# Kernel tuning notes

Measured on AMD Instinct MI355X. Metric: run time of the kernel, lower is better.

## Reference

```python
import jax, jax.numpy as jnp
import numpy as np

B, L, DG, H = 32, 1024, 1024, 1024  # batch, label_size (=n_graphs), graph dim, hidden

def setup_inputs() -> dict:
    key = jax.random.key(0)
    k1, k2, k3 = jax.random.split(key, 3)
    graph_repr = jax.random.normal(k1, (B, L, DG), dtype=jnp.float32)
    query = jax.random.normal(k2, (B, H), dtype=jnp.float32)
    W = jax.random.normal(k3, (H, L), dtype=jnp.float32) * (1.0 / np.sqrt(H))
    b = jnp.zeros((L,), dtype=jnp.float32)
    return {"graph_repr": graph_repr, "query": query, "W": W, "b": b}

def reference(graph_repr, query, W, b):
    # gate = Sigmoid(Linear(query)) : [B, L]
    gate = jax.nn.sigmoid(query @ W + b)
    # diag_embed(gate) @ graph_repr == per-row scale (same math, no O(L^2) matmul)
    scaled = gate[:, :, None] * graph_repr            # [B, L, DG]
    q_exp = jnp.broadcast_to(query[:, None, :], (query.shape[0], graph_repr.shape[1], query.shape[1]))
    return jnp.concatenate([scaled, q_exp], axis=-1)  # [B, L, DG+H]
```

## Files before the change

kernel.cpp:

```cpp
#include <hip/hip_runtime.h>

#define BB 32
#define LL 1024
#define DGG 1024
#define HH 1024

__global__ __launch_bounds__(256) void gate_kernel(
    const float* __restrict__ query,
    const float* __restrict__ W,
    const float* __restrict__ bias,
    float* __restrict__ gate)
{
    __shared__ float qs[HH];
    __shared__ float partial[4][64];

    const int b  = blockIdx.y;
    const int l0 = blockIdx.x * 64;
    const int t  = threadIdx.x;
    const int ll = t & 63;
    const int hg = t >> 6;

    for (int h = t; h < HH; h += 256)
        qs[h] = query[b * HH + h];
    __syncthreads();

    const int l = l0 + ll;
    const float* Wp = W + (size_t)(hg * 256) * LL + l;
    float sum = 0.f;
    #pragma unroll 8
    for (int h = 0; h < 256; ++h)
        sum += qs[hg * 256 + h] * Wp[(size_t)h * LL];

    partial[hg][ll] = sum;
    __syncthreads();

    if (t < 64) {
        float s = partial[0][t] + partial[1][t] + partial[2][t] + partial[3][t]
                + bias[l0 + t];
        gate[b * LL + l0 + t] = 1.0f / (1.0f + __expf(-s));
    }
}

__global__ __launch_bounds__(256) void out_kernel(
    const float* __restrict__ graph,
    const float* __restrict__ query,
    const float* __restrict__ gate,
    float* __restrict__ out)
{
    const int bl = blockIdx.x;
    const int b  = bl >> 10;
    const int t  = threadIdx.x;
    const float g = gate[bl];

    const float4* gsrc = reinterpret_cast<const float4*>(graph) + (size_t)bl * 256;
    const float4* qsrc = reinterpret_cast<const float4*>(query) + (size_t)b  * 256;
    float4*       dst  = reinterpret_cast<float4*>(out)         + (size_t)bl * 512;

    float4 v = gsrc[t];
    float4 r = make_float4(v.x * g, v.y * g, v.z * g, v.w * g);
    dst[t] = r;
    dst[256 + t] = qsrc[t];
}

extern "C" void kernel_launch(void* const* d_in, const int* in_sizes, int n_in,
                              void* d_out, int out_size, void* d_ws, size_t ws_size,
                              hipStream_t stream) {
    const float* graph = (const float*)d_in[0];
    const float* query = (const float*)d_in[1];
    const float* W     = (const float*)d_in[2];
    const float* bias  = (const float*)d_in[3];
    float* out  = (float*)d_out;
    float* gate = (float*)d_ws;

    dim3 g1(LL / 64, BB);
    gate_kernel<<<g1, 256, 0, stream>>>(query, W, bias, gate);
    out_kernel<<<BB * LL, 256, 0, stream>>>(graph, query, gate, out);
}
```

Before: 377.3 us.

## Fuse gate GEMV and scaled concat output into a single kernel

Merges the gate computation and the output write into one kernel: each block computes 16 gate values for one batch row in shared memory, then streams 16 graph rows, scales them and writes them along with the replicated query. This removes the second launch and the gate round-trip through global memory, and keeps query in registers for the concat half. In exchange, W is re-read per block with only 16-column-wide coalesced segments, and the GEMV is serialized in front of the streaming phase inside every block. Grid ordering puts batch on x, so blocks that share a W column slice run close together, which may help the W reads hit in cache.

After: 377.4 us. No clear change (+0.0%).

```diff
diff --git a/kernel.cpp b/kernel.cpp
--- a/kernel.cpp
+++ b/kernel.cpp
@@ -5,61 +5,56 @@
 #define DGG 1024
 #define HH 1024
 
-__global__ __launch_bounds__(256) void gate_kernel(
+__global__ __launch_bounds__(256) void fused_kernel(
+    const float* __restrict__ graph,
     const float* __restrict__ query,
     const float* __restrict__ W,
     const float* __restrict__ bias,
-    float* __restrict__ gate)
+    float* __restrict__ out)
 {
     __shared__ float qs[HH];
-    __shared__ float partial[4][64];
+    __shared__ float partial[16][16];
+    __shared__ float gate_s[16];
 
-    const int b  = blockIdx.y;
-    const int l0 = blockIdx.x * 64;
+    const int b  = blockIdx.x;
+    const int l0 = blockIdx.y * 16;
     const int t  = threadIdx.x;
-    const int ll = t & 63;
-    const int hg = t >> 6;
 
-    for (int h = t; h < HH; h += 256)
-        qs[h] = query[b * HH + h];
+    const float4* q4p = reinterpret_cast<const float4*>(query + (size_t)b * HH);
+    float4 q4 = q4p[t];
+    reinterpret_cast<float4*>(qs)[t] = q4;
     __syncthreads();
 
-    const int l = l0 + ll;
-    const float* Wp = W + (size_t)(hg * 256) * LL + l;
+    const int j  = t & 15;
+    const int hg = t >> 4;
+    const float* Wbase = W + l0 + j;
     float sum = 0.f;
     #pragma unroll 8
-    for (int h = 0; h < 256; ++h)
-        sum += qs[hg * 256 + h] * Wp[(size_t)h * LL];
-
-    partial[hg][ll] = sum;
+    for (int i = 0; i < 64; ++i) {
+        const int h = hg * 64 + ((i + hg * 4) & 63);
+        sum += qs[h] * Wbase[(size_t)h * LL];
+    }
+    partial[hg][j] = sum;
     __syncthreads();
 
-    if (t < 64) {
-        float s = partial[0][t] + partial[1][t] + partial[2][t] + partial[3][t]
-                + bias[l0 + t];
-        gate[b * LL + l0 + t] = 1.0f / (1.0f + __expf(-s));
+    if (t < 16) {
+        float s = bias[l0 + t];
+        #pragma unroll
+        for (int k = 0; k < 16; ++k) s += partial[k][t];
+        gate_s[t] = 1.0f / (1.0f + __expf(-s));
     }
-}
+    __syncthreads();
 
-__global__ __launch_bounds__(256) void out_kernel(
-    const float* __restrict__ graph,
-    const float* __restrict__ query,
-    const float* __restrict__ gate,
-    float* __restrict__ out)
-{
-    const int bl = blockIdx.x;
-    const int b  = bl >> 10;
-    const int t  = threadIdx.x;
-    const float g = gate[bl];
-
-    const float4* gsrc = reinterpret_cast<const float4*>(graph) + (size_t)bl * 256;
-    const float4* qsrc = reinterpret_cast<const float4*>(query) + (size_t)b  * 256;
-    float4*       dst  = reinterpret_cast<float4*>(out)         + (size_t)bl * 512;
-
-    float4 v = gsrc[t];
-    float4 r = make_float4(v.x * g, v.y * g, v.z * g, v.w * g);
-    dst[t] = r;
-    dst[256 + t] = qsrc[t];
+    const float4* g4 = reinterpret_cast<const float4*>(graph) + ((size_t)b * LL + l0) * 256;
+    float4*       o4 = reinterpret_cast<float4*>(out)         + ((size_t)b * LL + l0) * 512;
+    #pragma unroll 4
+    for (int r = 0; r < 16; ++r) {
+        const float g = gate_s[r];
+        float4 v = g4[(size_t)r * 256 + t];
+        float4 sv = make_float4(v.x * g, v.y * g, v.z * g, v.w * g);
+        o4[(size_t)r * 512 + t]       = sv;
+        o4[(size_t)r * 512 + 256 + t] = q4;
+    }
 }
 
 extern "C" void kernel_launch(void* const* d_in, const int* in_sizes, int n_in,
@@ -69,10 +64,8 @@
     const float* query = (const float*)d_in[1];
     const float* W     = (const float*)d_in[2];
     const float* bias  = (const float*)d_in[3];
-    float* out  = (float*)d_out;
-    float* gate = (float*)d_ws;
+    float* out = (float*)d_out;
 
-    dim3 g1(LL / 64, BB);
-    gate_kernel<<<g1, 256, 0, stream>>>(query, W, bias, gate);
-    out_kernel<<<BB * LL, 256, 0, stream>>>(graph, query, gate, out);
+    dim3 grid(BB, LL / 16);
+    fused_kernel<<<grid, 256, 0, stream>>>(graph, query, W, bias, out);
 }
```
